# Kernel tuning notes

Measured on AMD Instinct MI355X. Metric: run time of the kernel, lower is better.

Reference implementation:

```python
import jax, jax.numpy as jnp
import numpy as np

EPS = 1e-8  # torch F.cosine_similarity norm clamp


def setup_inputs() -> dict:
    key = jax.random.key(0)
    k1, k2, k3, k4 = jax.random.split(key, 4)
    B, N, M, D, T = 8, 4096, 2048, 512, 2
    return {
        "features": jax.random.normal(k1, (B, N, D), dtype=jnp.float32),
        "text": jax.random.normal(k2, (T, M, D), dtype=jnp.float32),
        "W": jax.random.normal(k3, (D, D), dtype=jnp.float32) * 0.02,
        "b": jax.random.normal(k4, (D,), dtype=jnp.float32) * 0.02,
    }


def reference(features, text, W, b):
    # features: [B, N, D] (output of the extractor), text: [T, M, D]
    B, N, D = features.shape
    f1 = jnp.einsum("bnd,de->bne", features, W) + b  # linear_layer(features)
    t1 = text[1]  # [M, D]; expanded across batch (row 1 per original code)

    # cosine similarity over last dim without materializing [B, N, M, D]
    fn = f1 / jnp.maximum(jnp.linalg.norm(f1, axis=-1, keepdims=True), EPS)
    tn = t1 / jnp.maximum(jnp.linalg.norm(t1, axis=-1, keepdims=True), EPS)
    sim = jnp.einsum("bnd,md->bnm", fn, tn)  # [B, N, M]

    e = jnp.exp(sim)
    w = e / jnp.sum(e, axis=1, keepdims=True)  # normalize over N (dim=1)

    # features_t [B,D,N] @ w [B,N,M] -> [B,D,M] -> transpose -> [B,M,D]
    fm = jnp.einsum("bnd,bnm->bmd", features, w)

    t1b = jnp.broadcast_to(t1[None, :, :], (B,) + t1.shape)  # [B, M, D]
    combine_feature = jnp.concatenate([fm, t1b], axis=2)  # [B, M, 2D]
    return combine_feature
```

## Files before the change

### kernel.cpp

```cpp
#include <hip/hip_runtime.h>

#define B_SZ 8
#define N_SZ 4096
#define M_SZ 2048
#define D_SZ 512

typedef __attribute__((ext_vector_type(8))) short bf16x8;
typedef __attribute__((ext_vector_type(4))) float f32x4;
typedef __attribute__((address_space(1))) const void* gptr1;
typedef __attribute__((address_space(3))) void* lptr3;

__device__ __forceinline__ unsigned short f2bf(float x) {
    unsigned int u = __builtin_bit_cast(unsigned int, x);
    u += 0x7fffu + ((u >> 16) & 1u);
    return (unsigned short)(u >> 16);
}
__device__ __forceinline__ float bf2f(unsigned short u) {
    unsigned int x = ((unsigned int)u) << 16;
    return __builtin_bit_cast(float, x);
}

__device__ __forceinline__ void vmcnt0() { asm volatile("s_waitcnt vmcnt(0)" ::: "memory"); }
__device__ __forceinline__ void vmcnt3() { asm volatile("s_waitcnt vmcnt(3)" ::: "memory"); }
__device__ __forceinline__ void vmcnt4() { asm volatile("s_waitcnt vmcnt(4)" ::: "memory"); }
template<int BN> __device__ __forceinline__ void vmcnt_steady() {
    if constexpr (BN == 256) vmcnt4(); else vmcnt3();
}

__device__ __forceinline__ void bt_mainloop(
    const unsigned short* __restrict__ A, const unsigned short* __restrict__ Bt,
    int lda, int ldb, int rowBase, int colBase, int K,
    unsigned short* As, unsigned short* Bs, f32x4 acc[4][4])
{
    const int tid  = threadIdx.x;
    const int lane = tid & 63;
    const int w    = tid >> 6;
    const int wr   = (w >> 1) * 64;
    const int wc   = (w & 1) * 64;
    const int lr   = lane & 15;
    const int kq   = lane >> 4;

    const int srow0 = w * 16 + (lane >> 2);
    const int skk   = (lane & 3) * 8;

    for (int k0 = 0; k0 < K; k0 += 32) {
#pragma unroll
        for (int j = 0; j < 2; ++j) {
            const unsigned short* ga = A  + (size_t)(rowBase + srow0 + j * 64) * lda + (k0 + skk);
            const unsigned short* gb = Bt + (size_t)(colBase + srow0 + j * 64) * ldb + (k0 + skk);
            __builtin_amdgcn_global_load_lds((gptr1)ga, (lptr3)(As + (j * 4 + w) * 512), 16, 0, 0);
            __builtin_amdgcn_global_load_lds((gptr1)gb, (lptr3)(Bs + (j * 4 + w) * 512), 16, 0, 0);
        }
        asm volatile("s_waitcnt vmcnt(0)" ::: "memory");
        __syncthreads();

        bf16x8 af[4], bq[4];
#pragma unroll
        for (int i = 0; i < 4; ++i) {
            af[i] = *(const bf16x8*)(As + (wr + i * 16 + lr) * 32 + kq * 8);
            bq[i] = *(const bf16x8*)(Bs + (wc + i * 16 + lr) * 32 + kq * 8);
        }
#pragma unroll
        for (int mi = 0; mi < 4; ++mi)
#pragma unroll
            for (int ni = 0; ni < 4; ++ni)
                acc[mi][ni] = __builtin_amdgcn_mfma_f32_16x16x32_bf16(af[mi], bq[ni], acc[mi][ni], 0, 0, 0);
        __syncthreads();
    }
}

template<int NROWS>
__device__ __forceinline__ void stage_half(
    const unsigned short* __restrict__ G, int ld, int grow0, int k0,
    unsigned short* lds, int tid)
{
    const int w = tid >> 6, l = tid & 63;
#pragma unroll
    for (int c = 0; c < NROWS / 64; ++c) {
        const int idx  = (c * 8 + w) * 64 + l;
        const int row  = idx >> 3;
        const int slot = (idx & 7) ^ (row & 7);
        const unsigned short* ga = G + (size_t)(grow0 + row) * ld + (k0 + slot * 8);
        __builtin_amdgcn_global_load_lds((gptr1)ga, (lptr3)(lds + (c * 8 + w) * 512), 16, 0, 0);
    }
}

#define PHASE(BUF, QM, QN, STAGES, TAIL)                                              \
  {                                                                                   \
    const unsigned short* Ab = As + (BUF) * (256 * 64);                               \
    const unsigned short* Bb = Bs + (BUF) * (BN * 64);                                \
    bf16x8 af[4][2], bq[NF2][2];                                                      \
    _Pragma("unroll") for (int mi = 0; mi < 4; ++mi)                                  \
      _Pragma("unroll") for (int ks = 0; ks < 2; ++ks) {                              \
        const int row = (QM) * 128 + wrow + mi * 16 + lr;                             \
        af[mi][ks] = *(const bf16x8*)(Ab + row * 64 + (((ks * 4 + kq) ^ (row & 7)) * 8)); \
      }                                                                               \
    _Pragma("unroll") for (int ni = 0; ni < NF2; ++ni)                                \
      _Pragma("unroll") for (int ks = 0; ks < 2; ++ks) {                              \
        const int row = (QN) * (BN / 2) + wcol + ni * 16 + lr;                        \
        bq[ni][ks] = *(const bf16x8*)(Bb + row * 64 + (((ks * 4 + kq) ^ (row & 7)) * 8)); \
      }                                                                               \
    STAGES;                                                                           \
    __builtin_amdgcn_s_barrier();                                                     \
    __builtin_amdgcn_s_setprio(1);                                                    \
    _Pragma("unroll") for (int mi = 0; mi < 4; ++mi)                                  \
      _Pragma("unroll") for (int ni = 0; ni < NF2; ++ni)                              \
        _Pragma("unroll") for (int ks = 0; ks < 2; ++ks)                              \
          acc[(QM) * 4 + mi][(QN) * NF2 + ni] = __builtin_amdgcn_mfma_f32_16x16x32_bf16( \
              af[mi][ks], bq[ni][ks], acc[(QM) * 4 + mi][(QN) * NF2 + ni], 0, 0, 0);  \
    __builtin_amdgcn_s_setprio(0);                                                    \
    TAIL;                                                                             \
    __builtin_amdgcn_s_barrier();                                                     \
  }

template<int BN>
__device__ __forceinline__ void mainloop8(
    const unsigned short* __restrict__ A, const unsigned short* __restrict__ Bt,
    int lda, int ldb, int rowBase, int colBase, int K,
    unsigned short* As, unsigned short* Bs, f32x4 (&acc)[8][BN / 64])
{
    constexpr int NF2  = BN / 128;
    constexpr int BNH  = BN / 2;
    constexpr int ABUF = 256 * 64, AH = 128 * 64;
    constexpr int BBUF = BN * 64,  BH = BNH * 64;
    const int tid = threadIdx.x, lane = tid & 63, w = tid >> 6;
    const int wrow = (w >> 2) * 64;
    const int wcol = (w & 3) * (BN / 8);
    const int lr = lane & 15, kq = lane >> 4;
    const int niter = K >> 7;

    stage_half<128>(A,  lda, rowBase,       0,  As,        tid);
    stage_half<BNH>(Bt, ldb, colBase,       0,  Bs,        tid);
    stage_half<128>(A,  lda, rowBase + 128, 0,  As + AH,   tid);
    stage_half<BNH>(Bt, ldb, colBase + BNH, 0,  Bs + BH,   tid);
    stage_half<128>(A,  lda, rowBase,       64, As + ABUF, tid);
    stage_half<BNH>(Bt, ldb, colBase,       64, Bs + BBUF, tid);
    vmcnt_steady<BN>();
    __builtin_amdgcn_s_barrier();

    for (int I = 0; I < niter; ++I) {
        const bool nl = (I + 1 < niter);
        const int ke = I << 7;
        PHASE(0, 0, 0, { stage_half<128>(A,  lda, rowBase + 128, ke + 64,  As + ABUF + AH, tid); }, {});
        PHASE(0, 0, 1, { stage_half<BNH>(Bt, ldb, colBase + BNH, ke + 64,  Bs + BBUF + BH, tid); }, {});
        PHASE(0, 1, 0, { if (nl) stage_half<128>(A,  lda, rowBase,       ke + 128, As,      tid); }, {});
        PHASE(0, 1, 1, { if (nl) stage_half<BNH>(Bt, ldb, colBase,       ke + 128, Bs,      tid); },
                       { if (nl) vmcnt_steady<BN>(); else vmcnt0(); });
        PHASE(1, 0, 0, { if (nl) stage_half<128>(A,  lda, rowBase + 128, ke + 128, As + AH, tid); }, {});
        PHASE(1, 0, 1, { if (nl) stage_half<BNH>(Bt, ldb, colBase + BNH, ke + 128, Bs + BH, tid); }, {});
        PHASE(1, 1, 0, { if (nl) stage_half<128>(A,  lda, rowBase,       ke + 192, As + ABUF, tid); }, {});
        PHASE(1, 1, 1, { if (nl) stage_half<BNH>(Bt, ldb, colBase,       ke + 192, Bs + BBUF, tid); },
                       { if (nl) vmcnt_steady<BN>(); else vmcnt0(); });
    }
}

__global__ __launch_bounds__(256) void prep_tn_k(
    const float* __restrict__ text, unsigned short* __restrict__ tn,
    float* __restrict__ out, float* __restrict__ L, float* __restrict__ SS)
{
    const int m = blockIdx.x;
    const int t = threadIdx.x;
    const float* t1 = text + (size_t)M_SZ * D_SZ;
    float2 v = ((const float2*)(t1 + (size_t)m * D_SZ))[t];
    float s = v.x * v.x + v.y * v.y;
#pragma unroll
    for (int off = 32; off > 0; off >>= 1) s += __shfl_down(s, off);
    __shared__ float partial[4];
    if ((t & 63) == 0) partial[t >> 6] = s;
    __syncthreads();
    float norm = sqrtf(partial[0] + partial[1] + partial[2] + partial[3]);
    norm = fmaxf(norm, 1e-8f);
    const float inv = 1.f / norm;
    ushort2 pk; pk.x = f2bf(v.x * inv); pk.y = f2bf(v.y * inv);
    ((ushort2*)(tn + (size_t)m * D_SZ))[t] = pk;
#pragma unroll
    for (int b = 0; b < B_SZ; ++b)
        ((float2*)(out + ((size_t)(b * M_SZ + m)) * (2 * D_SZ) + D_SZ))[t] = v;
    if (m < 64) L[m * 256 + t] = 0.f;
    if (m < 128) SS[m * 256 + t] = 0.f;
}

__global__ __launch_bounds__(256) void prep_w_k(
    const float* __restrict__ W, unsigned short* __restrict__ Wt)
{
    const int dt = blockIdx.x, et = blockIdx.y;
    const int t = threadIdx.x;
    __shared__ unsigned short tile[64][72];
    const int rr = t >> 4;
    const int cc = (t & 15) * 4;
#pragma unroll
    for (int p = 0; p < 4; ++p) {
        const int d = p * 16 + rr;
        const float4 v = *(const float4*)(W + (size_t)(dt * 64 + d) * D_SZ + et * 64 + cc);
        tile[d][cc] = f2bf(v.x); tile[d][cc + 1] = f2bf(v.y);
        tile[d][cc + 2] = f2bf(v.z); tile[d][cc + 3] = f2bf(v.w);
    }
    __syncthreads();
#pragma unroll
    for (int p = 0; p < 4; ++p) {
        const int e = p * 16 + rr;
        ushort4 pk;
        pk.x = tile[cc][e]; pk.y = tile[cc + 1][e]; pk.z = tile[cc + 2][e]; pk.w = tile[cc + 3][e];
        *(ushort4*)(Wt + (size_t)(et * 64 + e) * D_SZ + dt * 64 + cc) = pk;
    }
}

__global__ __launch_bounds__(256) void convert_feat_k(
    const float* __restrict__ feat, unsigned short* __restrict__ V,
    unsigned short* __restrict__ Vt)
{
    const int nt = blockIdx.x, dt = blockIdx.y, b = blockIdx.z;
    const int t = threadIdx.x;
    __shared__ unsigned short tile[64][72];
    const int rr = t >> 4;
    const int cc = (t & 15) * 4;
#pragma unroll
    for (int p = 0; p < 4; ++p) {
        const int r = p * 16 + rr;
        const size_t grow = (size_t)(b * N_SZ + nt * 64 + r);
        const float4 v = *(const float4*)(feat + grow * D_SZ + dt * 64 + cc);
        ushort4 pk; pk.x = f2bf(v.x); pk.y = f2bf(v.y); pk.z = f2bf(v.z); pk.w = f2bf(v.w);
        *(ushort4*)(V + grow * D_SZ + dt * 64 + cc) = pk;
        tile[r][cc] = pk.x; tile[r][cc + 1] = pk.y; tile[r][cc + 2] = pk.z; tile[r][cc + 3] = pk.w;
    }
    __syncthreads();
#pragma unroll
    for (int p = 0; p < 4; ++p) {
        const int d = p * 16 + rr;
        ushort4 pk;
        pk.x = tile[cc][d]; pk.y = tile[cc + 1][d]; pk.z = tile[cc + 2][d]; pk.w = tile[cc + 3][d];
        *(ushort4*)(Vt + ((size_t)(b * D_SZ + dt * 64 + d)) * N_SZ + nt * 64 + cc) = pk;
    }
}

__global__ __launch_bounds__(256) void gemm1_k(
    const unsigned short* __restrict__ V, const unsigned short* __restrict__ Wt,
    const float* __restrict__ bias, unsigned short* __restrict__ f1b,
    float* __restrict__ SS)
{
    __shared__ unsigned short As[128 * 32];
    __shared__ unsigned short Bs[128 * 32];
    f32x4 acc[4][4];
#pragma unroll
    for (int i = 0; i < 4; ++i)
#pragma unroll
        for (int j = 0; j < 4; ++j) acc[i][j] = (f32x4){0.f, 0.f, 0.f, 0.f};
    const int tid = threadIdx.x, lane = tid & 63, w = tid >> 6;
    const int wr = (w >> 1) * 64, wc = (w & 1) * 64, lr = lane & 15, kq = lane >> 4;

    const int rowBase = blockIdx.x * 128;
    const int colBase = blockIdx.y * 128;
    bt_mainloop(V, Wt, D_SZ, D_SZ, rowBase, colBase, D_SZ, As, Bs, acc);

#pragma unroll
    for (int mi = 0; mi < 4; ++mi) {
        const int r0 = rowBase + wr + mi * 16 + kq * 4;
        float s[4] = {0.f, 0.f, 0.f, 0.f};
#pragma unroll
        for (int ni = 0; ni < 4; ++ni) {
            const int c = colBase + wc + ni * 16 + lr;
            const float bv = bias[c];
#pragma unroll
            for (int r = 0; r < 4; ++r) {
                const float v = acc[mi][ni][r] + bv;
                f1b[(size_t)(r0 + r) * D_SZ + c] = f2bf(v);
                s[r] += v * v;
            }
        }
#pragma unroll
        for (int off = 1; off <= 8; off <<= 1)
#pragma unroll
            for (int r = 0; r < 4; ++r) s[r] += __shfl_xor(s[r], off);
        if (lr == 0) {
#pragma unroll
            for (int r = 0; r < 4; ++r) atomicAdd(&SS[r0 + r], s[r]);
        }
    }
}

__global__ __launch_bounds__(128) void normalize_k(
    const unsigned short* __restrict__ f1b, const float* __restrict__ SS,
    unsigned short* __restrict__ fn)
{
    const int row = blockIdx.x;
    const int t = threadIdx.x;
    const float norm = fmaxf(sqrtf(SS[row]), 1e-8f);
    const float inv = 1.f / norm;
    ushort4 v = ((const ushort4*)(f1b + (size_t)row * D_SZ))[t];
    ushort4 o;
    o.x = f2bf(bf2f(v.x) * inv); o.y = f2bf(bf2f(v.y) * inv);
    o.z = f2bf(bf2f(v.z) * inv); o.w = f2bf(bf2f(v.w) * inv);
    ((ushort4*)(fn + (size_t)row * D_SZ))[t] = o;
}

__global__ __launch_bounds__(512, 1) void gemm2_k8(
    const unsigned short* __restrict__ fn, const unsigned short* __restrict__ tn,
    unsigned short* __restrict__ E, float* __restrict__ L)
{
    __shared__ unsigned short smem[65536];
    unsigned short* As = smem;
    unsigned short* Bs = smem + 32768;
    f32x4 acc[8][4];
#pragma unroll
    for (int i = 0; i < 8; ++i)
#pragma unroll
        for (int j = 0; j < 4; ++j) acc[i][j] = (f32x4){0.f, 0.f, 0.f, 0.f};

    const int lin = blockIdx.x;
    const int xcd = lin & 7, slot = lin >> 3;
    const int mt = slot & 7;
    const int rt = (slot >> 3) * 8 + xcd;
    const int rowBase = rt * 256;
    const int colBase = mt * 256;

    mainloop8<256>(fn, tn, D_SZ, D_SZ, rowBase, colBase, D_SZ, As, Bs, acc);
    __syncthreads();

    const int tid = threadIdx.x, lane = tid & 63, w = tid >> 6;
    const int wrow = (w >> 2) * 64, wcol = (w & 3) * 32;
    const int lr = lane & 15, kq = lane >> 4;
    const int b = rowBase >> 12;
    const int nb0 = rowBase & 4095;

    unsigned short* P = smem;
    float ps[4] = {0.f, 0.f, 0.f, 0.f};
#pragma unroll
    for (int a = 0; a < 8; ++a) {
        const int n0 = (a >> 2) * 128 + wrow + (a & 3) * 16 + kq * 4;
#pragma unroll
        for (int j = 0; j < 4; ++j) {
            const int m = (j >> 1) * 128 + wcol + (j & 1) * 16 + lr;
            const float e0 = __expf(acc[a][j][0]);
            const float e1 = __expf(acc[a][j][1]);
            const float e2 = __expf(acc[a][j][2]);
            const float e3 = __expf(acc[a][j][3]);
            ushort4 pk; pk.x = f2bf(e0); pk.y = f2bf(e1); pk.z = f2bf(e2); pk.w = f2bf(e3);
            *(ushort4*)(P + m * 256 + (((n0 >> 3) ^ (m & 7)) * 8) + (n0 & 7)) = pk;
            ps[j] += (e0 + e1) + (e2 + e3);
        }
    }
#pragma unroll
    for (int j = 0; j < 4; ++j) {
        float p = ps[j];
        p += __shfl_down(p, 16);
        p += __shfl_down(p, 32);
        const int m = (j >> 1) * 128 + wcol + (j & 1) * 16 + lr;
        if (lane < 16) atomicAdd(&L[b * M_SZ + colBase + m], p);
    }
    __syncthreads();

    unsigned short* Eb = E + (size_t)b * M_SZ * N_SZ;
#pragma unroll
    for (int c = 0; c < 16; ++c) {
        const int rm = c * 16 + (tid >> 5);
        const int ns = tid & 31;
        bf16x8 v = *(const bf16x8*)(P + rm * 256 + ((ns ^ (rm & 7)) * 8));
        *(bf16x8*)(Eb + (size_t)(colBase + rm) * N_SZ + nb0 + ns * 8) = v;
    }
}

__global__ __launch_bounds__(512, 1) void gemm3_k8(
    const unsigned short* __restrict__ E, const unsigned short* __restrict__ Vt,
    const float* __restrict__ L, float* __restrict__ out)
{
    __shared__ unsigned short smem[49152];
    unsigned short* As = smem;
    unsigned short* Bs = smem + 32768;
    f32x4 acc[8][2];
#pragma unroll
    for (int i = 0; i < 8; ++i)
#pragma unroll
        for (int j = 0; j < 2; ++j) acc[i][j] = (f32x4){0.f, 0.f, 0.f, 0.f};

    const int lin = blockIdx.x;
    const int mtile = lin & 7;
    const int slot = lin >> 3;
    const int dt = slot & 3;
    const int b = slot >> 2;
    const int rowBase = mtile * 256;
    const int colBase = dt * 128;

    const unsigned short* Ab = E + (size_t)b * M_SZ * N_SZ;
    const unsigned short* Bb = Vt + (size_t)b * D_SZ * N_SZ;
    mainloop8<128>(Ab, Bb, N_SZ, N_SZ, rowBase, colBase, N_SZ, As, Bs, acc);

    const int tid = threadIdx.x, lane = tid & 63, w = tid >> 6;
    const int wrow = (w >> 2) * 64, wcol = (w & 3) * 16;
    const int lr = lane & 15, kq = lane >> 4;

#pragma unroll
    for (int a = 0; a < 8; ++a) {
        const int r0 = rowBase + (a >> 2) * 128 + wrow + (a & 3) * 16 + kq * 4;
        float invl[4];
#pragma unroll
        for (int r = 0; r < 4; ++r) invl[r] = 1.f / L[b * M_SZ + r0 + r];
#pragma unroll
        for (int j = 0; j < 2; ++j) {
            const int d = colBase + j * 64 + wcol + lr;
#pragma unroll
            for (int r = 0; r < 4; ++r)
                out[((size_t)(b * M_SZ + r0 + r)) * (2 * D_SZ) + d] = acc[a][j][r] * invl[r];
        }
    }
}

extern "C" void kernel_launch(void* const* d_in, const int* in_sizes, int n_in,
                              void* d_out, int out_size, void* d_ws, size_t ws_size,
                              hipStream_t stream) {
    const float* features = (const float*)d_in[0];
    const float* text     = (const float*)d_in[1];
    const float* W        = (const float*)d_in[2];
    const float* bias     = (const float*)d_in[3];
    float* out = (float*)d_out;
    char* ws = (char*)d_ws;

    unsigned short* fn  = (unsigned short*)(ws + 0);
    unsigned short* tn  = (unsigned short*)(ws + 33554432);
    unsigned short* Wt  = (unsigned short*)(ws + 35651584);
    unsigned short* V   = (unsigned short*)(ws + 36175872);
    unsigned short* Vt  = (unsigned short*)(ws + 69730304);
    float*          L   = (float*)(ws + 103284736);
    float*          SS  = (float*)(ws + 103350272);
    unsigned short* E   = (unsigned short*)(ws + 103481344);
    unsigned short* f1b = (unsigned short*)(ws + 103481344);

    hipLaunchKernelGGL(prep_tn_k, dim3(M_SZ), dim3(256), 0, stream, text, tn, out, L, SS);
    hipLaunchKernelGGL(prep_w_k, dim3(8, 8), dim3(256), 0, stream, W, Wt);
    hipLaunchKernelGGL(convert_feat_k, dim3(64, 8, 8), dim3(256), 0, stream, features, V, Vt);
    hipLaunchKernelGGL(gemm1_k, dim3(256, 4), dim3(256), 0, stream, V, Wt, bias, f1b, SS);
    hipLaunchKernelGGL(normalize_k, dim3(32768), dim3(128), 0, stream, f1b, SS, fn);
    hipLaunchKernelGGL(gemm2_k8, dim3(1024), dim3(512), 0, stream, fn, tn, E, L);
    hipLaunchKernelGGL(gemm3_k8, dim3(256), dim3(512), 0, stream, E, Vt, L, out);
}
```

Baseline: 367.8 us.

## Restructure GEMM mainloop from eight to four phases per K-iteration

Each K-tile is now split into four phases instead of eight: each phase covers one A half and both B halves, loading the full B fragment set and issuing twice the MFMAs per barrier pair. The global-to-LDS staging schedule is reorganized so that the B halves are prefetched together with an A half, and the wait counts are adjusted to match. This halves the number of barriers and phase boundaries in both GEMMs. In exchange, each phase holds more B fragments in registers, and the loads are grouped more coarsely, which may expose more memory latency.

```diff
diff --git a/kernel.cpp b/kernel.cpp
--- a/kernel.cpp
+++ b/kernel.cpp
@@ -21,11 +21,7 @@
 }
 
 __device__ __forceinline__ void vmcnt0() { asm volatile("s_waitcnt vmcnt(0)" ::: "memory"); }
-__device__ __forceinline__ void vmcnt3() { asm volatile("s_waitcnt vmcnt(3)" ::: "memory"); }
-__device__ __forceinline__ void vmcnt4() { asm volatile("s_waitcnt vmcnt(4)" ::: "memory"); }
-template<int BN> __device__ __forceinline__ void vmcnt_steady() {
-    if constexpr (BN == 256) vmcnt4(); else vmcnt3();
-}
+__device__ __forceinline__ void vmcnt2() { asm volatile("s_waitcnt vmcnt(2)" ::: "memory"); }
 
 __device__ __forceinline__ void bt_mainloop(
     const unsigned short* __restrict__ A, const unsigned short* __restrict__ Bt,
@@ -85,41 +81,41 @@
     }
 }
 
-#define PHASE(BUF, QM, QN, STAGES, TAIL)                                              \
+#define PHASE4(BUF, QM, STAGES, TAIL)                                                 \
   {                                                                                   \
     const unsigned short* Ab = As + (BUF) * (256 * 64);                               \
     const unsigned short* Bb = Bs + (BUF) * (BN * 64);                                \
-    bf16x8 af[4][2], bq[NF2][2];                                                      \
+    bf16x8 af[4][2], bq[NF][2];                                                       \
+    _Pragma("unroll") for (int nj = 0; nj < NF; ++nj)                                 \
+      _Pragma("unroll") for (int ks = 0; ks < 2; ++ks) {                              \
+        const int row = (nj / (NF / 2)) * (BN / 2) + wcol + (nj % (NF / 2)) * 16 + lr; \
+        bq[nj][ks] = *(const bf16x8*)(Bb + row * 64 + (((ks * 4 + kq) ^ (row & 7)) * 8)); \
+      }                                                                               \
     _Pragma("unroll") for (int mi = 0; mi < 4; ++mi)                                  \
       _Pragma("unroll") for (int ks = 0; ks < 2; ++ks) {                              \
         const int row = (QM) * 128 + wrow + mi * 16 + lr;                             \
         af[mi][ks] = *(const bf16x8*)(Ab + row * 64 + (((ks * 4 + kq) ^ (row & 7)) * 8)); \
       }                                                                               \
-    _Pragma("unroll") for (int ni = 0; ni < NF2; ++ni)                                \
-      _Pragma("unroll") for (int ks = 0; ks < 2; ++ks) {                              \
-        const int row = (QN) * (BN / 2) + wcol + ni * 16 + lr;                        \
-        bq[ni][ks] = *(const bf16x8*)(Bb + row * 64 + (((ks * 4 + kq) ^ (row & 7)) * 8)); \
-      }                                                                               \
     STAGES;                                                                           \
     __builtin_amdgcn_s_barrier();                                                     \
     __builtin_amdgcn_s_setprio(1);                                                    \
     _Pragma("unroll") for (int mi = 0; mi < 4; ++mi)                                  \
-      _Pragma("unroll") for (int ni = 0; ni < NF2; ++ni)                              \
+      _Pragma("unroll") for (int nj = 0; nj < NF; ++nj)                               \
         _Pragma("unroll") for (int ks = 0; ks < 2; ++ks)                              \
-          acc[(QM) * 4 + mi][(QN) * NF2 + ni] = __builtin_amdgcn_mfma_f32_16x16x32_bf16( \
-              af[mi][ks], bq[ni][ks], acc[(QM) * 4 + mi][(QN) * NF2 + ni], 0, 0, 0);  \
+          acc[(QM) * 4 + mi][nj] = __builtin_amdgcn_mfma_f32_16x16x32_bf16(           \
+              af[mi][ks], bq[nj][ks], acc[(QM) * 4 + mi][nj], 0, 0, 0);               \
     __builtin_amdgcn_s_setprio(0);                                                    \
     TAIL;                                                                             \
     __builtin_amdgcn_s_barrier();                                                     \
   }
 
 template<int BN>
-__device__ __forceinline__ void mainloop8(
+__device__ __forceinline__ void mainloop4(
     const unsigned short* __restrict__ A, const unsigned short* __restrict__ Bt,
     int lda, int ldb, int rowBase, int colBase, int K,
     unsigned short* As, unsigned short* Bs, f32x4 (&acc)[8][BN / 64])
 {
-    constexpr int NF2  = BN / 128;
+    constexpr int NF   = BN / 64;
     constexpr int BNH  = BN / 2;
     constexpr int ABUF = 256 * 64, AH = 128 * 64;
     constexpr int BBUF = BN * 64,  BH = BNH * 64;
@@ -130,27 +126,32 @@
     const int niter = K >> 7;
 
     stage_half<128>(A,  lda, rowBase,       0,  As,        tid);
+    stage_half<128>(A,  lda, rowBase + 128, 0,  As + AH,   tid);
     stage_half<BNH>(Bt, ldb, colBase,       0,  Bs,        tid);
-    stage_half<128>(A,  lda, rowBase + 128, 0,  As + AH,   tid);
     stage_half<BNH>(Bt, ldb, colBase + BNH, 0,  Bs + BH,   tid);
     stage_half<128>(A,  lda, rowBase,       64, As + ABUF, tid);
-    stage_half<BNH>(Bt, ldb, colBase,       64, Bs + BBUF, tid);
-    vmcnt_steady<BN>();
+    vmcnt2();
     __builtin_amdgcn_s_barrier();
 
     for (int I = 0; I < niter; ++I) {
         const bool nl = (I + 1 < niter);
         const int ke = I << 7;
-        PHASE(0, 0, 0, { stage_half<128>(A,  lda, rowBase + 128, ke + 64,  As + ABUF + AH, tid); }, {});
-        PHASE(0, 0, 1, { stage_half<BNH>(Bt, ldb, colBase + BNH, ke + 64,  Bs + BBUF + BH, tid); }, {});
-        PHASE(0, 1, 0, { if (nl) stage_half<128>(A,  lda, rowBase,       ke + 128, As,      tid); }, {});
-        PHASE(0, 1, 1, { if (nl) stage_half<BNH>(Bt, ldb, colBase,       ke + 128, Bs,      tid); },
-                       { if (nl) vmcnt_steady<BN>(); else vmcnt0(); });
-        PHASE(1, 0, 0, { if (nl) stage_half<128>(A,  lda, rowBase + 128, ke + 128, As + AH, tid); }, {});
-        PHASE(1, 0, 1, { if (nl) stage_half<BNH>(Bt, ldb, colBase + BNH, ke + 128, Bs + BH, tid); }, {});
-        PHASE(1, 1, 0, { if (nl) stage_half<128>(A,  lda, rowBase,       ke + 192, As + ABUF, tid); }, {});
-        PHASE(1, 1, 1, { if (nl) stage_half<BNH>(Bt, ldb, colBase,       ke + 192, Bs + BBUF, tid); },
-                       { if (nl) vmcnt_steady<BN>(); else vmcnt0(); });
+        PHASE4(0, 0,
+          { stage_half<128>(A,  lda, rowBase + 128, ke + 64, As + ABUF + AH, tid);
+            stage_half<BNH>(Bt, ldb, colBase,       ke + 64, Bs + BBUF,      tid);
+            stage_half<BNH>(Bt, ldb, colBase + BNH, ke + 64, Bs + BBUF + BH, tid); },
+          {});
+        PHASE4(0, 1,
+          { if (nl) stage_half<128>(A, lda, rowBase, ke + 128, As, tid); },
+          { if (nl) vmcnt2(); else vmcnt0(); });
+        PHASE4(1, 0,
+          { if (nl) { stage_half<128>(A,  lda, rowBase + 128, ke + 128, As + AH, tid);
+                      stage_half<BNH>(Bt, ldb, colBase,       ke + 128, Bs,      tid);
+                      stage_half<BNH>(Bt, ldb, colBase + BNH, ke + 128, Bs + BH, tid); } },
+          {});
+        PHASE4(1, 1,
+          { if (nl) stage_half<128>(A, lda, rowBase, ke + 192, As + ABUF, tid); },
+          { if (nl) vmcnt2(); });
     }
 }
 
@@ -313,7 +314,7 @@
     const int rowBase = rt * 256;
     const int colBase = mt * 256;
 
-    mainloop8<256>(fn, tn, D_SZ, D_SZ, rowBase, colBase, D_SZ, As, Bs, acc);
+    mainloop4<256>(fn, tn, D_SZ, D_SZ, rowBase, colBase, D_SZ, As, Bs, acc);
     __syncthreads();
 
     const int tid = threadIdx.x, lane = tid & 63, w = tid >> 6;
@@ -382,7 +383,7 @@
 
     const unsigned short* Ab = E + (size_t)b * M_SZ * N_SZ;
     const unsigned short* Bb = Vt + (size_t)b * D_SZ * N_SZ;
-    mainloop8<128>(Ab, Bb, N_SZ, N_SZ, rowBase, colBase, N_SZ, As, Bs, acc);
+    mainloop4<128>(Ab, Bb, N_SZ, N_SZ, rowBase, colBase, N_SZ, As, Bs, acc);
 
     const int tid = threadIdx.x, lane = tid & 63, w = tid >> 6;
     const int wrow = (w >> 2) * 64, wcol = (w & 3) * 16;
```

Result: slower. 376.2 us (+2.3%).

## Fold row normalization into gemm2 epilogue and move gemm1 to pipelined mainloop

Applied to the files above, without the earlier changes.

Removes the separate normalize kernel. gemm2 now reads the unnormalized f1 and scales each dot product by the inverse row norm, computed from SS in shared memory, before the exp. gemm1 moves from the simple single-buffered 128x128 loop to the 8-wave pipelined mainloop8 with 256x256 tiles. The final vmcnt0 drain in the last iteration is dropped, and gemm3's block-index mapping is reordered so batch varies fastest. Normalizing after the bf16 GEMM rather than before changes rounding slightly, and the removed drain depends on no loads being outstanding at the end.

```diff
diff --git a/kernel.cpp b/kernel.cpp
--- a/kernel.cpp
+++ b/kernel.cpp
@@ -25,48 +25,6 @@
 __device__ __forceinline__ void vmcnt4() { asm volatile("s_waitcnt vmcnt(4)" ::: "memory"); }
 template<int BN> __device__ __forceinline__ void vmcnt_steady() {
     if constexpr (BN == 256) vmcnt4(); else vmcnt3();
-}
-
-__device__ __forceinline__ void bt_mainloop(
-    const unsigned short* __restrict__ A, const unsigned short* __restrict__ Bt,
-    int lda, int ldb, int rowBase, int colBase, int K,
-    unsigned short* As, unsigned short* Bs, f32x4 acc[4][4])
-{
-    const int tid  = threadIdx.x;
-    const int lane = tid & 63;
-    const int w    = tid >> 6;
-    const int wr   = (w >> 1) * 64;
-    const int wc   = (w & 1) * 64;
-    const int lr   = lane & 15;
-    const int kq   = lane >> 4;
-
-    const int srow0 = w * 16 + (lane >> 2);
-    const int skk   = (lane & 3) * 8;
-
-    for (int k0 = 0; k0 < K; k0 += 32) {
-#pragma unroll
-        for (int j = 0; j < 2; ++j) {
-            const unsigned short* ga = A  + (size_t)(rowBase + srow0 + j * 64) * lda + (k0 + skk);
-            const unsigned short* gb = Bt + (size_t)(colBase + srow0 + j * 64) * ldb + (k0 + skk);
-            __builtin_amdgcn_global_load_lds((gptr1)ga, (lptr3)(As + (j * 4 + w) * 512), 16, 0, 0);
-            __builtin_amdgcn_global_load_lds((gptr1)gb, (lptr3)(Bs + (j * 4 + w) * 512), 16, 0, 0);
-        }
-        asm volatile("s_waitcnt vmcnt(0)" ::: "memory");
-        __syncthreads();
-
-        bf16x8 af[4], bq[4];
-#pragma unroll
-        for (int i = 0; i < 4; ++i) {
-            af[i] = *(const bf16x8*)(As + (wr + i * 16 + lr) * 32 + kq * 8);
-            bq[i] = *(const bf16x8*)(Bs + (wc + i * 16 + lr) * 32 + kq * 8);
-        }
-#pragma unroll
-        for (int mi = 0; mi < 4; ++mi)
-#pragma unroll
-            for (int ni = 0; ni < 4; ++ni)
-                acc[mi][ni] = __builtin_amdgcn_mfma_f32_16x16x32_bf16(af[mi], bq[ni], acc[mi][ni], 0, 0, 0);
-        __syncthreads();
-    }
 }
 
 template<int NROWS>
@@ -150,7 +108,7 @@
         PHASE(1, 0, 1, { if (nl) stage_half<BNH>(Bt, ldb, colBase + BNH, ke + 128, Bs + BH, tid); }, {});
         PHASE(1, 1, 0, { if (nl) stage_half<128>(A,  lda, rowBase,       ke + 192, As + ABUF, tid); }, {});
         PHASE(1, 1, 1, { if (nl) stage_half<BNH>(Bt, ldb, colBase,       ke + 192, Bs + BBUF, tid); },
-                       { if (nl) vmcnt_steady<BN>(); else vmcnt0(); });
+                       { if (nl) vmcnt_steady<BN>(); });
     }
 }
 
@@ -233,37 +191,47 @@
     }
 }
 
-__global__ __launch_bounds__(256) void gemm1_k(
+__global__ __launch_bounds__(512, 1) void gemm1_k8(
     const unsigned short* __restrict__ V, const unsigned short* __restrict__ Wt,
     const float* __restrict__ bias, unsigned short* __restrict__ f1b,
     float* __restrict__ SS)
 {
-    __shared__ unsigned short As[128 * 32];
-    __shared__ unsigned short Bs[128 * 32];
-    f32x4 acc[4][4];
-#pragma unroll
-    for (int i = 0; i < 4; ++i)
+    __shared__ unsigned short smem[65536];
+    unsigned short* As = smem;
+    unsigned short* Bs = smem + 32768;
+    f32x4 acc[8][4];
+#pragma unroll
+    for (int i = 0; i < 8; ++i)
 #pragma unroll
         for (int j = 0; j < 4; ++j) acc[i][j] = (f32x4){0.f, 0.f, 0.f, 0.f};
+
+    const int lin = blockIdx.x;
+    const int rowBase = (lin >> 1) * 256;
+    const int colBase = (lin & 1) * 256;
+
+    mainloop8<256>(V, Wt, D_SZ, D_SZ, rowBase, colBase, D_SZ, As, Bs, acc);
+
     const int tid = threadIdx.x, lane = tid & 63, w = tid >> 6;
-    const int wr = (w >> 1) * 64, wc = (w & 1) * 64, lr = lane & 15, kq = lane >> 4;
-
-    const int rowBase = blockIdx.x * 128;
-    const int colBase = blockIdx.y * 128;
-    bt_mainloop(V, Wt, D_SZ, D_SZ, rowBase, colBase, D_SZ, As, Bs, acc);
-
-#pragma unroll
-    for (int mi = 0; mi < 4; ++mi) {
-        const int r0 = rowBase + wr + mi * 16 + kq * 4;
+    const int wrow = (w >> 2) * 64, wcol = (w & 3) * 32;
+    const int lr = lane & 15, kq = lane >> 4;
+
+    float bv[4];
+    int cs[4];
+#pragma unroll
+    for (int j = 0; j < 4; ++j) {
+        cs[j] = colBase + (j >> 1) * 128 + wcol + (j & 1) * 16 + lr;
+        bv[j] = bias[cs[j]];
+    }
+#pragma unroll
+    for (int a = 0; a < 8; ++a) {
+        const int r0 = rowBase + (a >> 2) * 128 + wrow + (a & 3) * 16 + kq * 4;
         float s[4] = {0.f, 0.f, 0.f, 0.f};
 #pragma unroll
-        for (int ni = 0; ni < 4; ++ni) {
-            const int c = colBase + wc + ni * 16 + lr;
-            const float bv = bias[c];
+        for (int j = 0; j < 4; ++j) {
 #pragma unroll
             for (int r = 0; r < 4; ++r) {
-                const float v = acc[mi][ni][r] + bv;
-                f1b[(size_t)(r0 + r) * D_SZ + c] = f2bf(v);
+                const float v = acc[a][j][r] + bv[j];
+                f1b[(size_t)(r0 + r) * D_SZ + cs[j]] = f2bf(v);
                 s[r] += v * v;
             }
         }
@@ -278,26 +246,13 @@
     }
 }
 
-__global__ __launch_bounds__(128) void normalize_k(
-    const unsigned short* __restrict__ f1b, const float* __restrict__ SS,
-    unsigned short* __restrict__ fn)
-{
-    const int row = blockIdx.x;
-    const int t = threadIdx.x;
-    const float norm = fmaxf(sqrtf(SS[row]), 1e-8f);
-    const float inv = 1.f / norm;
-    ushort4 v = ((const ushort4*)(f1b + (size_t)row * D_SZ))[t];
-    ushort4 o;
-    o.x = f2bf(bf2f(v.x) * inv); o.y = f2bf(bf2f(v.y) * inv);
-    o.z = f2bf(bf2f(v.z) * inv); o.w = f2bf(bf2f(v.w) * inv);
-    ((ushort4*)(fn + (size_t)row * D_SZ))[t] = o;
-}
-
 __global__ __launch_bounds__(512, 1) void gemm2_k8(
-    const unsigned short* __restrict__ fn, const unsigned short* __restrict__ tn,
-    unsigned short* __restrict__ E, float* __restrict__ L)
+    const unsigned short* __restrict__ f1b, const unsigned short* __restrict__ tn,
+    const float* __restrict__ SS, unsigned short* __restrict__ E,
+    float* __restrict__ L)
 {
     __shared__ unsigned short smem[65536];
+    __shared__ float invn[256];
     unsigned short* As = smem;
     unsigned short* Bs = smem + 32768;
     f32x4 acc[8][4];
@@ -313,10 +268,15 @@
     const int rowBase = rt * 256;
     const int colBase = mt * 256;
 
-    mainloop8<256>(fn, tn, D_SZ, D_SZ, rowBase, colBase, D_SZ, As, Bs, acc);
-    __syncthreads();
+    mainloop8<256>(f1b, tn, D_SZ, D_SZ, rowBase, colBase, D_SZ, As, Bs, acc);
 
     const int tid = threadIdx.x, lane = tid & 63, w = tid >> 6;
+    if (tid < 256) {
+        const float ss = SS[rowBase + tid];
+        invn[tid] = 1.f / fmaxf(sqrtf(ss), 1e-8f);
+    }
+    __syncthreads();
+
     const int wrow = (w >> 2) * 64, wcol = (w & 3) * 32;
     const int lr = lane & 15, kq = lane >> 4;
     const int b = rowBase >> 12;
@@ -327,13 +287,14 @@
 #pragma unroll
     for (int a = 0; a < 8; ++a) {
         const int n0 = (a >> 2) * 128 + wrow + (a & 3) * 16 + kq * 4;
+        const float4 inr = *(const float4*)(invn + n0);
 #pragma unroll
         for (int j = 0; j < 4; ++j) {
             const int m = (j >> 1) * 128 + wcol + (j & 1) * 16 + lr;
-            const float e0 = __expf(acc[a][j][0]);
-            const float e1 = __expf(acc[a][j][1]);
-            const float e2 = __expf(acc[a][j][2]);
-            const float e3 = __expf(acc[a][j][3]);
+            const float e0 = __expf(acc[a][j][0] * inr.x);
+            const float e1 = __expf(acc[a][j][1] * inr.y);
+            const float e2 = __expf(acc[a][j][2] * inr.z);
+            const float e3 = __expf(acc[a][j][3] * inr.w);
             ushort4 pk; pk.x = f2bf(e0); pk.y = f2bf(e1); pk.z = f2bf(e2); pk.w = f2bf(e3);
             *(ushort4*)(P + m * 256 + (((n0 >> 3) ^ (m & 7)) * 8) + (n0 & 7)) = pk;
             ps[j] += (e0 + e1) + (e2 + e3);
@@ -373,10 +334,9 @@
         for (int j = 0; j < 2; ++j) acc[i][j] = (f32x4){0.f, 0.f, 0.f, 0.f};
 
     const int lin = blockIdx.x;
-    const int mtile = lin & 7;
-    const int slot = lin >> 3;
-    const int dt = slot & 3;
-    const int b = slot >> 2;
+    const int b = lin & 7;
+    const int mtile = (lin >> 3) & 7;
+    const int dt = lin >> 6;
     const int rowBase = mtile * 256;
     const int colBase = dt * 128;
 
@@ -414,7 +374,7 @@
     float* out = (float*)d_out;
     char* ws = (char*)d_ws;
 
-    unsigned short* fn  = (unsigned short*)(ws + 0);
+    unsigned short* f1b = (unsigned short*)(ws + 0);
     unsigned short* tn  = (unsigned short*)(ws + 33554432);
     unsigned short* Wt  = (unsigned short*)(ws + 35651584);
     unsigned short* V   = (unsigned short*)(ws + 36175872);
@@ -422,13 +382,11 @@
     float*          L   = (float*)(ws + 103284736);
     float*          SS  = (float*)(ws + 103350272);
     unsigned short* E   = (unsigned short*)(ws + 103481344);
-    unsigned short* f1b = (unsigned short*)(ws + 103481344);
 
     hipLaunchKernelGGL(prep_tn_k, dim3(M_SZ), dim3(256), 0, stream, text, tn, out, L, SS);
     hipLaunchKernelGGL(prep_w_k, dim3(8, 8), dim3(256), 0, stream, W, Wt);
     hipLaunchKernelGGL(convert_feat_k, dim3(64, 8, 8), dim3(256), 0, stream, features, V, Vt);
-    hipLaunchKernelGGL(gemm1_k, dim3(256, 4), dim3(256), 0, stream, V, Wt, bias, f1b, SS);
-    hipLaunchKernelGGL(normalize_k, dim3(32768), dim3(128), 0, stream, f1b, SS, fn);
-    hipLaunchKernelGGL(gemm2_k8, dim3(1024), dim3(512), 0, stream, fn, tn, E, L);
+    hipLaunchKernelGGL(gemm1_k8, dim3(256), dim3(512), 0, stream, V, Wt, bias, f1b, SS);
+    hipLaunchKernelGGL(gemm2_k8, dim3(1024), dim3(512), 0, stream, f1b, tn, SS, E, L);
     hipLaunchKernelGGL(gemm3_k8, dim3(256), dim3(512), 0, stream, E, Vt, L, out);
 }
```

Result: faster. 358.7 us (-2.5%).
